# Optimization experiments

Hardware: AMD Instinct MI355X
Metric: run time of the kernel (lower is better)

Reference implementation:

```python
import jax, jax.numpy as jnp
import numpy as np

H = 1024        # hidden_size
E = 3           # num_smear experts
DI = 1280       # int(1.25 * H), GRU inner dim (expansion_factor=1.25)
EPS = 1e-6


def setup_inputs() -> dict:
    key = jax.random.key(0)
    ks = jax.random.split(key, 5)
    B, S = 4, 4096
    s = 0.02
    return {
        "inputs": jax.random.normal(ks[0], (B, S, H), jnp.float32),
        "norm_weight": jnp.ones((H,), jnp.float32),
        "router_w": jax.random.normal(ks[1], (H, E), jnp.float32) * s,
        "router_b": jnp.zeros((E,), jnp.float32),
        "w_in": jax.random.normal(ks[2], (E, H, 2 * DI), jnp.float32) * s,
        "b_in": jnp.zeros((E, 2 * DI), jnp.float32),
        "w_out": jax.random.normal(ks[3], (E, DI, H), jnp.float32) * s,
        "b_out": jnp.zeros((E, H), jnp.float32),
    }


def _g(x):
    # minGRU candidate activation: x + 0.5 for x >= 0, sigmoid(x) otherwise
    return jnp.where(x >= 0, x + 0.5, jax.nn.sigmoid(x))


def reference(inputs, norm_weight, router_w, router_b, w_in, b_in, w_out, b_out):
    B, S, _ = inputs.shape
    # RMSNorm
    x = inputs * jax.lax.rsqrt(jnp.mean(inputs * inputs, axis=-1, keepdims=True) + EPS)
    x = x * norm_weight

    # SMEAR routing: softmax over experts from mean-pooled tokens, per sample
    pooled = x.mean(axis=1)                                   # [B, H]
    probs = jax.nn.softmax(pooled @ router_w + router_b, -1)  # [B, E]

    # Soft-merge expert parameters per sample
    Wi = jnp.einsum('be,edh->bdh', probs, w_in)    # [B, H, 2*DI]
    bi = jnp.einsum('be,eh->bh', probs, b_in)      # [B, 2*DI]
    Wo = jnp.einsum('be,edh->bdh', probs, w_out)   # [B, DI, H]
    bo = jnp.einsum('be,eh->bh', probs, b_out)     # [B, H]

    # GRU (minGRU) input projection
    zh = jnp.einsum('bsd,bdh->bsh', x, Wi) + bi[:, None, :]   # [B, S, 2*DI]
    hid, gate = jnp.split(zh, 2, axis=-1)
    z = jax.nn.sigmoid(gate)   # update gate [B, S, DI]
    ht = _g(hid)               # candidate    [B, S, DI]

    def step(h, zt_ht):
        z_t, ht_t = zt_ht
        h = (1.0 - z_t) * h + z_t * ht_t
        return h, h

    h0 = jnp.zeros((B, DI), x.dtype)
    _, hs = jax.lax.scan(step, h0, (z.swapaxes(0, 1), ht.swapaxes(0, 1)))
    hs = hs.swapaxes(0, 1)     # [B, S, DI]

    out = jnp.einsum('bsh,bhd->bsd', hs, Wo) + bo[:, None, :]  # proj_out
    out = out + inputs                                          # residual (dropout=0, eval)
    new_state = hs[:, -1]                                       # [B, DI]
    aux_loss = jnp.zeros((), inputs.dtype)
    return out, new_state, aux_loss
```

## Files before the change

kernel.cpp:

```cpp
#include <hip/hip_runtime.h>
#include <hip/hip_bf16.h>

#define B_  4
#define S_  4096
#define H_  1024
#define DI_ 1280
#define DI2_ 2560
#define E_  3
#define NC_ 64
#define CL_ 64
#define EPS_ 1e-6f

typedef unsigned short ushort_t;
typedef __attribute__((ext_vector_type(8))) __bf16 bf16x8;
typedef __attribute__((ext_vector_type(4))) float f32x4;

__device__ inline ushort_t f2bf(float f) {
    union { float f; unsigned u; } v; v.f = f;
    unsigned r = v.u + 0x7fffu + ((v.u >> 16) & 1u);
    return (ushort_t)(r >> 16);
}
__device__ inline float bf2f(ushort_t s) {
    union { unsigned u; float f; } v; v.u = ((unsigned)s) << 16;
    return v.f;
}
__device__ inline float sigmoidf_(float x) { return 1.0f / (1.0f + __expf(-x)); }

__device__ inline void gld16(const void* g, void* l) {
    __builtin_amdgcn_global_load_lds(
        (const __attribute__((address_space(1))) void*)g,
        (__attribute__((address_space(3))) void*)l, 16, 0, 0);
}

__global__ __launch_bounds__(256) void rmsnorm_kernel(
    const float* __restrict__ in, const float* __restrict__ nw,
    ushort_t* __restrict__ xbf, float* __restrict__ partial)
{
    int g = blockIdx.x, b = blockIdx.y;
    int tid = threadIdx.x, lane = tid & 63, w = tid >> 6;
    int s0 = g * 16;
    const float4* inb = (const float4*)(in + ((size_t)b * S_ + s0) * H_);
    float4 rows[16];
    float ss[16];
#pragma unroll
    for (int r = 0; r < 16; r++) {
        float4 v = inb[(size_t)r * (H_ / 4) + tid];
        rows[r] = v;
        ss[r] = v.x * v.x + v.y * v.y + v.z * v.z + v.w * v.w;
    }
#pragma unroll
    for (int r = 0; r < 16; r++) {
        float s = ss[r];
        s += __shfl_down(s, 32); s += __shfl_down(s, 16); s += __shfl_down(s, 8);
        s += __shfl_down(s, 4);  s += __shfl_down(s, 2);  s += __shfl_down(s, 1);
        ss[r] = s;
    }
    __shared__ float red[16][4];
    __shared__ float scl[16];
    if (lane == 0) {
#pragma unroll
        for (int r = 0; r < 16; r++) red[r][w] = ss[r];
    }
    __syncthreads();
    if (tid < 16) {
        float t = red[tid][0] + red[tid][1] + red[tid][2] + red[tid][3];
        scl[tid] = rsqrtf(t * (1.0f / H_) + EPS_);
    }
    __syncthreads();
    float4 nw4 = ((const float4*)nw)[tid];
    float4 pacc = {0.f, 0.f, 0.f, 0.f};
    ushort_t* xrow = xbf + ((size_t)b * S_ + s0) * H_;
#pragma unroll
    for (int r = 0; r < 16; r++) {
        float sc = scl[r];
        float4 v = rows[r];
        v.x = v.x * sc * nw4.x; v.y = v.y * sc * nw4.y;
        v.z = v.z * sc * nw4.z; v.w = v.w * sc * nw4.w;
        ushort4 u; u.x = f2bf(v.x); u.y = f2bf(v.y); u.z = f2bf(v.z); u.w = f2bf(v.w);
        *(ushort4*)(xrow + (size_t)r * H_ + tid * 4) = u;
        pacc.x += v.x; pacc.y += v.y; pacc.z += v.z; pacc.w += v.w;
    }
    float4* pp = (float4*)(partial + ((size_t)(b * 256 + g)) * H_);
    pp[tid] = pacc;
}

__global__ __launch_bounds__(256) void router_kernel(
    const float* __restrict__ partial, const float* __restrict__ rw,
    const float* __restrict__ rb, const float* __restrict__ b_in,
    const float* __restrict__ b_out, float* __restrict__ probs,
    float* __restrict__ bi, float* __restrict__ bo, float* __restrict__ aux)
{
    int b = blockIdx.x;
    int tid = threadIdx.x, lane = tid & 63, w = tid >> 6;
    float4 acc = {0.f, 0.f, 0.f, 0.f};
    const float4* pp = (const float4*)partial;
    for (int g = 0; g < 256; g++) {
        float4 v = pp[((size_t)(b * 256 + g)) * (H_ / 4) + tid];
        acc.x += v.x; acc.y += v.y; acc.z += v.z; acc.w += v.w;
    }
    const float inv_s = 1.0f / (float)S_;
    float a4[4] = {acc.x * inv_s, acc.y * inv_s, acc.z * inv_s, acc.w * inv_s};
    float le[3] = {0.f, 0.f, 0.f};
    int h0 = tid * 4;
#pragma unroll
    for (int j = 0; j < 4; j++) {
        float p = a4[j];
        le[0] += p * rw[(size_t)(h0 + j) * 3 + 0];
        le[1] += p * rw[(size_t)(h0 + j) * 3 + 1];
        le[2] += p * rw[(size_t)(h0 + j) * 3 + 2];
    }
#pragma unroll
    for (int e = 0; e < 3; e++) {
        float s = le[e];
        s += __shfl_down(s, 32); s += __shfl_down(s, 16); s += __shfl_down(s, 8);
        s += __shfl_down(s, 4);  s += __shfl_down(s, 2);  s += __shfl_down(s, 1);
        le[e] = s;
    }
    __shared__ float red[4][3];
    __shared__ float pr[3];
    if (lane == 0) { red[w][0] = le[0]; red[w][1] = le[1]; red[w][2] = le[2]; }
    __syncthreads();
    if (tid == 0) {
        float l0 = red[0][0] + red[1][0] + red[2][0] + red[3][0] + rb[0];
        float l1 = red[0][1] + red[1][1] + red[2][1] + red[3][1] + rb[1];
        float l2 = red[0][2] + red[1][2] + red[2][2] + red[3][2] + rb[2];
        float m = fmaxf(l0, fmaxf(l1, l2));
        float e0 = __expf(l0 - m), e1 = __expf(l1 - m), e2 = __expf(l2 - m);
        float inv = 1.0f / (e0 + e1 + e2);
        pr[0] = e0 * inv; pr[1] = e1 * inv; pr[2] = e2 * inv;
    }
    __syncthreads();
    if (tid < 3) probs[b * 3 + tid] = pr[tid];
    float p0 = pr[0], p1 = pr[1], p2 = pr[2];
    for (int n = tid; n < DI2_; n += 256)
        bi[(size_t)b * DI2_ + n] = p0 * b_in[n] + p1 * b_in[DI2_ + n] + p2 * b_in[2 * DI2_ + n];
    for (int n = tid; n < H_; n += 256)
        bo[(size_t)b * H_ + n] = p0 * b_out[n] + p1 * b_out[H_ + n] + p2 * b_out[2 * H_ + n];
    if (b == 0 && tid == 0) *aux = 0.0f;
}

__global__ __launch_bounds__(256) void mix_kernel(
    const float* __restrict__ wsrc, const float* __restrict__ probs,
    ushort_t* __restrict__ dst, int K, int N)
{
    int kt = blockIdx.x, nt = blockIdx.y, b = blockIdx.z;
    float p0 = probs[b * 3 + 0], p1 = probs[b * 3 + 1], p2 = probs[b * 3 + 2];
    __shared__ float T[64][65];
    int tid = threadIdx.x;
    int c = tid & 63, rr = tid >> 6;
    const float* w0 = wsrc;
    const float* w1 = wsrc + (size_t)K * N;
    const float* w2 = wsrc + 2 * (size_t)K * N;
    int k0 = kt * 64, n0 = nt * 64;
#pragma unroll
    for (int pass = 0; pass < 16; pass++) {
        int r = pass * 4 + rr;
        size_t idx = (size_t)(k0 + r) * N + n0 + c;
        T[r][c] = p0 * w0[idx] + p1 * w1[idx] + p2 * w2[idx];
    }
    __syncthreads();
    ushort_t* db = dst + (size_t)b * N * K;
#pragma unroll
    for (int pass = 0; pass < 16; pass++) {
        int j = pass * 4 + rr;
        db[(size_t)(n0 + j) * K + k0 + c] = f2bf(T[c][j]);
    }
}

template <int MODE>
__global__ __launch_bounds__(256, 2) void gemm_bt(
    const ushort_t* __restrict__ Aall, const ushort_t* __restrict__ Btall,
    int M, int N, int K,
    const float* __restrict__ biasAll,
    const float* __restrict__ resAll, float* __restrict__ outAll,
    ushort_t* __restrict__ htAll, ushort_t* __restrict__ zAll, int DIv)
{
    __shared__ ushort_t As[128 * 32];
    __shared__ ushort_t Bs[128 * 32];
    int b = blockIdx.z;
    const ushort_t* A = Aall + (size_t)b * M * K;
    const ushort_t* Bt = Btall + (size_t)b * N * K;
    int tid = threadIdx.x, lane = tid & 63, w = tid >> 6;
    int mblk = blockIdx.x * 128, nblk = blockIdx.y * 128;

    int srow = lane >> 2;
    int scol = (lane & 3) * 8;
    const ushort_t* ga0 = A + (size_t)(mblk + (w * 2 + 0) * 16 + srow) * K + scol;
    const ushort_t* ga1 = A + (size_t)(mblk + (w * 2 + 1) * 16 + srow) * K + scol;
    const ushort_t* gb0 = Bt + (size_t)(nblk + (w * 2 + 0) * 16 + srow) * K + scol;
    const ushort_t* gb1 = Bt + (size_t)(nblk + (w * 2 + 1) * 16 + srow) * K + scol;
    ushort_t* la0 = &As[(w * 2 + 0) * 512 + lane * 8];
    ushort_t* la1 = &As[(w * 2 + 1) * 512 + lane * 8];
    ushort_t* lb0 = &Bs[(w * 2 + 0) * 512 + lane * 8];
    ushort_t* lb1 = &Bs[(w * 2 + 1) * 512 + lane * 8];

    f32x4 acc[4][4] = {};
    int wy = w & 1, wx = w >> 1;
    int q = lane >> 4;
    int ml = lane & 15;
    int aoff0 = (wy * 64 + ml) * 32 + q * 8;
    int boff0 = (wx * 64 + ml) * 32 + q * 8;

    for (int k0 = 0; k0 < K; k0 += 32) {
        gld16(ga0, la0); gld16(ga1, la1);
        gld16(gb0, lb0); gld16(gb1, lb1);
        ga0 += 32; ga1 += 32; gb0 += 32; gb1 += 32;
        __syncthreads();
        bf16x8 af[4], bfr[4];
#pragma unroll
        for (int i = 0; i < 4; i++) af[i] = *(const bf16x8*)&As[aoff0 + i * 16 * 32];
#pragma unroll
        for (int i = 0; i < 4; i++) bfr[i] = *(const bf16x8*)&Bs[boff0 + i * 16 * 32];
#pragma unroll
        for (int mi = 0; mi < 4; mi++)
#pragma unroll
            for (int ni = 0; ni < 4; ni++)
                acc[mi][ni] = __builtin_amdgcn_mfma_f32_16x16x32_bf16(af[mi], bfr[ni], acc[mi][ni], 0, 0, 0);
        __syncthreads();
    }

    int mbase = mblk + wy * 64 + q * 4;
    int nbase = nblk + wx * 64 + ml;
    const float* bias = biasAll + (size_t)b * N;
    if (MODE == 0) {
        bool isgate = (nblk >= DIv);
        ushort_t* dst = (isgate ? zAll : htAll) + (size_t)b * (size_t)M * DIv;
#pragma unroll
        for (int ni = 0; ni < 4; ni++) {
            int n = nbase + ni * 16;
            float bv = bias[n];
            int ncol = isgate ? (n - DIv) : n;
#pragma unroll
            for (int mi = 0; mi < 4; mi++) {
                int m = mbase + mi * 16;
#pragma unroll
                for (int r = 0; r < 4; r++) {
                    float v = acc[mi][ni][r] + bv;
                    float res;
                    if (isgate) res = sigmoidf_(v);
                    else res = (v >= 0.f) ? (v + 0.5f) : sigmoidf_(v);
                    dst[(size_t)(m + r) * DIv + ncol] = f2bf(res);
                }
            }
        }
    } else {
        const float* resb = resAll + (size_t)b * (size_t)M * N;
        float* outp = outAll + (size_t)b * (size_t)M * N;
#pragma unroll
        for (int ni = 0; ni < 4; ni++) {
            int n = nbase + ni * 16;
            float bv = bias[n];
#pragma unroll
            for (int mi = 0; mi < 4; mi++) {
                int m = mbase + mi * 16;
#pragma unroll
                for (int r = 0; r < 4; r++) {
                    size_t idx = (size_t)(m + r) * N + n;
                    outp[idx] = acc[mi][ni][r] + bv + resb[idx];
                }
            }
        }
    }
}

__global__ __launch_bounds__(256) void scan_phase1(
    const ushort_t* __restrict__ zb, const ushort_t* __restrict__ hb,
    float* __restrict__ cA, float* __restrict__ cB)
{
    int d = blockIdx.x * 256 + threadIdx.x;
    int c = blockIdx.y, b = blockIdx.z;
    size_t base = ((size_t)b * S_ + (size_t)c * CL_) * DI_ + d;
    float A = 1.f, Bc = 0.f;
    for (int t = 0; t < CL_; t++) {
        float z = bf2f(zb[base + (size_t)t * DI_]);
        float h = bf2f(hb[base + (size_t)t * DI_]);
        float a = 1.f - z;
        A *= a;
        Bc = a * Bc + z * h;
    }
    size_t o = ((size_t)b * NC_ + c) * DI_ + d;
    cA[o] = A;
    cB[o] = Bc;
}

__global__ __launch_bounds__(256) void scan_phase2(
    const float* __restrict__ cA, const float* __restrict__ cB,
    float* __restrict__ h0buf, float* __restrict__ ns)
{
    int g = blockIdx.x * 256 + threadIdx.x;
    int b = g / DI_, d = g % DI_;
    float h = 0.f;
    for (int c = 0; c < NC_; c++) {
        size_t o = ((size_t)b * NC_ + c) * DI_ + d;
        h0buf[o] = h;
        h = cA[o] * h + cB[o];
    }
    ns[(size_t)b * DI_ + d] = h;
}

__global__ __launch_bounds__(256) void scan_phase3(
    const ushort_t* __restrict__ zb, const ushort_t* __restrict__ hb,
    const float* __restrict__ h0buf, ushort_t* __restrict__ hs)
{
    int d = blockIdx.x * 256 + threadIdx.x;
    int c = blockIdx.y, b = blockIdx.z;
    size_t base = ((size_t)b * S_ + (size_t)c * CL_) * DI_ + d;
    float h = h0buf[((size_t)b * NC_ + c) * DI_ + d];
    for (int t = 0; t < CL_; t++) {
        float z = bf2f(zb[base + (size_t)t * DI_]);
        float ht = bf2f(hb[base + (size_t)t * DI_]);
        h = (1.f - z) * h + z * ht;
        hs[base + (size_t)t * DI_] = f2bf(h);
    }
}

extern "C" void kernel_launch(void* const* d_in, const int* in_sizes, int n_in,
                              void* d_out, int out_size, void* d_ws, size_t ws_size,
                              hipStream_t stream)
{
    const float* in    = (const float*)d_in[0];
    const float* nw    = (const float*)d_in[1];
    const float* rw    = (const float*)d_in[2];
    const float* rb    = (const float*)d_in[3];
    const float* w_in  = (const float*)d_in[4];
    const float* b_in  = (const float*)d_in[5];
    const float* w_out = (const float*)d_in[6];
    const float* b_out = (const float*)d_in[7];
    float* out = (float*)d_out;

    char* ws = (char*)d_ws;
    size_t off = 0;
    auto nxt = [&](size_t bytes) -> void* {
        void* p = ws + off;
        off += (bytes + 255) & ~(size_t)255;
        return p;
    };
    ushort_t* xbf    = (ushort_t*)nxt((size_t)B_ * S_ * H_ * 2);
    ushort_t* wi_t   = (ushort_t*)nxt((size_t)B_ * DI2_ * H_ * 2);
    ushort_t* wo_t   = (ushort_t*)nxt((size_t)B_ * H_ * DI_ * 2);
    ushort_t* zbuf   = (ushort_t*)nxt((size_t)B_ * S_ * DI_ * 2);
    ushort_t* htbuf  = (ushort_t*)nxt((size_t)B_ * S_ * DI_ * 2);
    ushort_t* hsbuf  = (ushort_t*)nxt((size_t)B_ * S_ * DI_ * 2);
    float* partial   = (float*)nxt((size_t)B_ * 256 * H_ * 4);
    float* probs     = (float*)nxt((size_t)B_ * 3 * 4);
    float* bi        = (float*)nxt((size_t)B_ * DI2_ * 4);
    float* bo        = (float*)nxt((size_t)B_ * H_ * 4);
    float* cA        = (float*)nxt((size_t)B_ * NC_ * DI_ * 4);
    float* cB        = (float*)nxt((size_t)B_ * NC_ * DI_ * 4);
    float* h0buf     = (float*)nxt((size_t)B_ * NC_ * DI_ * 4);

    float* ns  = out + (size_t)B_ * S_ * H_;
    float* aux = ns + (size_t)B_ * DI_;

    rmsnorm_kernel<<<dim3(S_ / 16, B_), 256, 0, stream>>>(in, nw, xbf, partial);
    router_kernel<<<dim3(B_), 256, 0, stream>>>(partial, rw, rb, b_in, b_out, probs, bi, bo, aux);
    mix_kernel<<<dim3(H_ / 64, DI2_ / 64, B_), 256, 0, stream>>>(w_in, probs, wi_t, H_, DI2_);
    mix_kernel<<<dim3(DI_ / 64, H_ / 64, B_), 256, 0, stream>>>(w_out, probs, wo_t, DI_, H_);
    gemm_bt<0><<<dim3(S_ / 128, DI2_ / 128, B_), 256, 0, stream>>>(
        xbf, wi_t, S_, DI2_, H_, bi, nullptr, nullptr, htbuf, zbuf, DI_);
    scan_phase1<<<dim3(DI_ / 256, NC_, B_), 256, 0, stream>>>(zbuf, htbuf, cA, cB);
    scan_phase2<<<dim3((B_ * DI_) / 256), 256, 0, stream>>>(cA, cB, h0buf, ns);
    scan_phase3<<<dim3(DI_ / 256, NC_, B_), 256, 0, stream>>>(zbuf, htbuf, h0buf, hsbuf);
    gemm_bt<1><<<dim3(S_ / 128, H_ / 128, B_), 256, 0, stream>>>(
        hsbuf, wo_t, S_, H_, DI_, bo, in, out, nullptr, nullptr, DI_);
    (void)in_sizes; (void)n_in; (void)out_size; (void)ws_size;
}
```

Measured before the change: 463.7 us.

## Swizzle GEMM LDS layout, vectorize epilogue stores and scan kernels

The GEMM stages its shared-memory tiles with an XOR swizzle to avoid bank conflicts. It also swaps the MFMA operand order so each lane holds four consecutive output columns, which lets the epilogue use vector stores for the bf16 and fp32 outputs and vector loads for the residual and bias. The three scan phases now process four channels per thread with vector loads and stores, using fewer, wider blocks. The scan grids shrink, so phase2 runs only 5 blocks and phases 1 and 3 run 256 blocks, which may leave much of the GPU idle.

```diff
diff --git a/kernel.cpp b/kernel.cpp
--- a/kernel.cpp
+++ b/kernel.cpp
@@ -184,7 +184,8 @@
     int mblk = blockIdx.x * 128, nblk = blockIdx.y * 128;
 
     int srow = lane >> 2;
-    int scol = (lane & 3) * 8;
+    int sblk = (lane & 3) ^ ((srow >> 1) & 3);
+    int scol = sblk * 8;
     const ushort_t* ga0 = A + (size_t)(mblk + (w * 2 + 0) * 16 + srow) * K + scol;
     const ushort_t* ga1 = A + (size_t)(mblk + (w * 2 + 1) * 16 + srow) * K + scol;
     const ushort_t* gb0 = Bt + (size_t)(nblk + (w * 2 + 0) * 16 + srow) * K + scol;
@@ -198,8 +199,9 @@
     int wy = w & 1, wx = w >> 1;
     int q = lane >> 4;
     int ml = lane & 15;
-    int aoff0 = (wy * 64 + ml) * 32 + q * 8;
-    int boff0 = (wx * 64 + ml) * 32 + q * 8;
+    int rblk = (q ^ ((ml >> 1) & 3)) * 8;
+    int aoff0 = wy * 2048 + ml * 32 + rblk;
+    int boff0 = wx * 2048 + ml * 32 + rblk;
 
     for (int k0 = 0; k0 < K; k0 += 32) {
         gld16(ga0, la0); gld16(ga1, la1);
@@ -208,79 +210,94 @@
         __syncthreads();
         bf16x8 af[4], bfr[4];
 #pragma unroll
-        for (int i = 0; i < 4; i++) af[i] = *(const bf16x8*)&As[aoff0 + i * 16 * 32];
-#pragma unroll
-        for (int i = 0; i < 4; i++) bfr[i] = *(const bf16x8*)&Bs[boff0 + i * 16 * 32];
+        for (int i = 0; i < 4; i++) af[i] = *(const bf16x8*)&As[aoff0 + i * 512];
+#pragma unroll
+        for (int i = 0; i < 4; i++) bfr[i] = *(const bf16x8*)&Bs[boff0 + i * 512];
 #pragma unroll
         for (int mi = 0; mi < 4; mi++)
 #pragma unroll
             for (int ni = 0; ni < 4; ni++)
-                acc[mi][ni] = __builtin_amdgcn_mfma_f32_16x16x32_bf16(af[mi], bfr[ni], acc[mi][ni], 0, 0, 0);
+                acc[mi][ni] = __builtin_amdgcn_mfma_f32_16x16x32_bf16(bfr[ni], af[mi], acc[mi][ni], 0, 0, 0);
         __syncthreads();
     }
 
-    int mbase = mblk + wy * 64 + q * 4;
-    int nbase = nblk + wx * 64 + ml;
+    int nq = nblk + wx * 64 + q * 4;
     const float* bias = biasAll + (size_t)b * N;
     if (MODE == 0) {
         bool isgate = (nblk >= DIv);
         ushort_t* dst = (isgate ? zAll : htAll) + (size_t)b * (size_t)M * DIv;
-#pragma unroll
-        for (int ni = 0; ni < 4; ni++) {
-            int n = nbase + ni * 16;
-            float bv = bias[n];
-            int ncol = isgate ? (n - DIv) : n;
-#pragma unroll
-            for (int mi = 0; mi < 4; mi++) {
-                int m = mbase + mi * 16;
-#pragma unroll
-                for (int r = 0; r < 4; r++) {
-                    float v = acc[mi][ni][r] + bv;
-                    float res;
-                    if (isgate) res = sigmoidf_(v);
-                    else res = (v >= 0.f) ? (v + 0.5f) : sigmoidf_(v);
-                    dst[(size_t)(m + r) * DIv + ncol] = f2bf(res);
+        int ncol0 = isgate ? (nq - DIv) : nq;
+#pragma unroll
+        for (int mi = 0; mi < 4; mi++) {
+            int m = mblk + wy * 64 + mi * 16 + ml;
+            ushort_t* drow = dst + (size_t)m * DIv;
+#pragma unroll
+            for (int ni = 0; ni < 4; ni++) {
+                float4 bv = *(const float4*)&bias[nq + ni * 16];
+                f32x4 a = acc[mi][ni];
+                float v0 = a[0] + bv.x, v1 = a[1] + bv.y, v2 = a[2] + bv.z, v3 = a[3] + bv.w;
+                float r0, r1, r2, r3;
+                if (isgate) {
+                    r0 = sigmoidf_(v0); r1 = sigmoidf_(v1); r2 = sigmoidf_(v2); r3 = sigmoidf_(v3);
+                } else {
+                    r0 = (v0 >= 0.f) ? (v0 + 0.5f) : sigmoidf_(v0);
+                    r1 = (v1 >= 0.f) ? (v1 + 0.5f) : sigmoidf_(v1);
+                    r2 = (v2 >= 0.f) ? (v2 + 0.5f) : sigmoidf_(v2);
+                    r3 = (v3 >= 0.f) ? (v3 + 0.5f) : sigmoidf_(v3);
                 }
+                ushort4 u; u.x = f2bf(r0); u.y = f2bf(r1); u.z = f2bf(r2); u.w = f2bf(r3);
+                *(ushort4*)&drow[ncol0 + ni * 16] = u;
             }
         }
     } else {
         const float* resb = resAll + (size_t)b * (size_t)M * N;
         float* outp = outAll + (size_t)b * (size_t)M * N;
 #pragma unroll
-        for (int ni = 0; ni < 4; ni++) {
-            int n = nbase + ni * 16;
-            float bv = bias[n];
-#pragma unroll
-            for (int mi = 0; mi < 4; mi++) {
-                int m = mbase + mi * 16;
-#pragma unroll
-                for (int r = 0; r < 4; r++) {
-                    size_t idx = (size_t)(m + r) * N + n;
-                    outp[idx] = acc[mi][ni][r] + bv + resb[idx];
-                }
+        for (int mi = 0; mi < 4; mi++) {
+            int m = mblk + wy * 64 + mi * 16 + ml;
+            const float* rrow = resb + (size_t)m * N;
+            float* orow = outp + (size_t)m * N;
+#pragma unroll
+            for (int ni = 0; ni < 4; ni++) {
+                int n0 = nq + ni * 16;
+                float4 bv = *(const float4*)&bias[n0];
+                float4 rv = *(const float4*)&rrow[n0];
+                f32x4 a = acc[mi][ni];
+                float4 o;
+                o.x = a[0] + bv.x + rv.x; o.y = a[1] + bv.y + rv.y;
+                o.z = a[2] + bv.z + rv.z; o.w = a[3] + bv.w + rv.w;
+                *(float4*)&orow[n0] = o;
             }
         }
     }
 }
 
-__global__ __launch_bounds__(256) void scan_phase1(
+__global__ __launch_bounds__(320) void scan_phase1(
     const ushort_t* __restrict__ zb, const ushort_t* __restrict__ hb,
     float* __restrict__ cA, float* __restrict__ cB)
 {
-    int d = blockIdx.x * 256 + threadIdx.x;
-    int c = blockIdx.y, b = blockIdx.z;
-    size_t base = ((size_t)b * S_ + (size_t)c * CL_) * DI_ + d;
-    float A = 1.f, Bc = 0.f;
+    int d0 = threadIdx.x * 4;
+    int c = blockIdx.x, b = blockIdx.y;
+    size_t base = ((size_t)b * S_ + (size_t)c * CL_) * DI_ + d0;
+    float A[4] = {1.f, 1.f, 1.f, 1.f};
+    float Bc[4] = {0.f, 0.f, 0.f, 0.f};
     for (int t = 0; t < CL_; t++) {
-        float z = bf2f(zb[base + (size_t)t * DI_]);
-        float h = bf2f(hb[base + (size_t)t * DI_]);
-        float a = 1.f - z;
-        A *= a;
-        Bc = a * Bc + z * h;
-    }
-    size_t o = ((size_t)b * NC_ + c) * DI_ + d;
-    cA[o] = A;
-    cB[o] = Bc;
+        ushort4 zv = *(const ushort4*)&zb[base + (size_t)t * DI_];
+        ushort4 hv = *(const ushort4*)&hb[base + (size_t)t * DI_];
+        float z[4] = {bf2f(zv.x), bf2f(zv.y), bf2f(zv.z), bf2f(zv.w)};
+        float h[4] = {bf2f(hv.x), bf2f(hv.y), bf2f(hv.z), bf2f(hv.w)};
+#pragma unroll
+        for (int j = 0; j < 4; j++) {
+            float a = 1.f - z[j];
+            A[j] *= a;
+            Bc[j] = a * Bc[j] + z[j] * h[j];
+        }
+    }
+    size_t o = ((size_t)b * NC_ + c) * DI_ + d0;
+    float4 av; av.x = A[0]; av.y = A[1]; av.z = A[2]; av.w = A[3];
+    float4 bv; bv.x = Bc[0]; bv.y = Bc[1]; bv.z = Bc[2]; bv.w = Bc[3];
+    *(float4*)&cA[o] = av;
+    *(float4*)&cB[o] = bv;
 }
 
 __global__ __launch_bounds__(256) void scan_phase2(
@@ -288,29 +305,40 @@
     float* __restrict__ h0buf, float* __restrict__ ns)
 {
     int g = blockIdx.x * 256 + threadIdx.x;
-    int b = g / DI_, d = g % DI_;
-    float h = 0.f;
+    int b = g / (DI_ / 4), dq = g % (DI_ / 4);
+    int d0 = dq * 4;
+    float4 h = {0.f, 0.f, 0.f, 0.f};
     for (int c = 0; c < NC_; c++) {
-        size_t o = ((size_t)b * NC_ + c) * DI_ + d;
-        h0buf[o] = h;
-        h = cA[o] * h + cB[o];
-    }
-    ns[(size_t)b * DI_ + d] = h;
-}
-
-__global__ __launch_bounds__(256) void scan_phase3(
+        size_t o = ((size_t)b * NC_ + c) * DI_ + d0;
+        *(float4*)&h0buf[o] = h;
+        float4 a = *(const float4*)&cA[o];
+        float4 bb = *(const float4*)&cB[o];
+        h.x = a.x * h.x + bb.x; h.y = a.y * h.y + bb.y;
+        h.z = a.z * h.z + bb.z; h.w = a.w * h.w + bb.w;
+    }
+    *(float4*)&ns[(size_t)b * DI_ + d0] = h;
+}
+
+__global__ __launch_bounds__(320) void scan_phase3(
     const ushort_t* __restrict__ zb, const ushort_t* __restrict__ hb,
     const float* __restrict__ h0buf, ushort_t* __restrict__ hs)
 {
-    int d = blockIdx.x * 256 + threadIdx.x;
-    int c = blockIdx.y, b = blockIdx.z;
-    size_t base = ((size_t)b * S_ + (size_t)c * CL_) * DI_ + d;
-    float h = h0buf[((size_t)b * NC_ + c) * DI_ + d];
+    int d0 = threadIdx.x * 4;
+    int c = blockIdx.x, b = blockIdx.y;
+    size_t base = ((size_t)b * S_ + (size_t)c * CL_) * DI_ + d0;
+    float4 h0 = *(const float4*)&h0buf[((size_t)b * NC_ + c) * DI_ + d0];
+    float h[4] = {h0.x, h0.y, h0.z, h0.w};
     for (int t = 0; t < CL_; t++) {
-        float z = bf2f(zb[base + (size_t)t * DI_]);
-        float ht = bf2f(hb[base + (size_t)t * DI_]);
-        h = (1.f - z) * h + z * ht;
-        hs[base + (size_t)t * DI_] = f2bf(h);
+        ushort4 zv = *(const ushort4*)&zb[base + (size_t)t * DI_];
+        ushort4 hv = *(const ushort4*)&hb[base + (size_t)t * DI_];
+        float z[4] = {bf2f(zv.x), bf2f(zv.y), bf2f(zv.z), bf2f(zv.w)};
+        float ht[4] = {bf2f(hv.x), bf2f(hv.y), bf2f(hv.z), bf2f(hv.w)};
+        ushort4 u;
+        h[0] = (1.f - z[0]) * h[0] + z[0] * ht[0]; u.x = f2bf(h[0]);
+        h[1] = (1.f - z[1]) * h[1] + z[1] * ht[1]; u.y = f2bf(h[1]);
+        h[2] = (1.f - z[2]) * h[2] + z[2] * ht[2]; u.z = f2bf(h[2]);
+        h[3] = (1.f - z[3]) * h[3] + z[3] * ht[3]; u.w = f2bf(h[3]);
+        *(ushort4*)&hs[base + (size_t)t * DI_] = u;
     }
 }
 
@@ -358,9 +386,9 @@
     mix_kernel<<<dim3(DI_ / 64, H_ / 64, B_), 256, 0, stream>>>(w_out, probs, wo_t, DI_, H_);
     gemm_bt<0><<<dim3(S_ / 128, DI2_ / 128, B_), 256, 0, stream>>>(
         xbf, wi_t, S_, DI2_, H_, bi, nullptr, nullptr, htbuf, zbuf, DI_);
-    scan_phase1<<<dim3(DI_ / 256, NC_, B_), 256, 0, stream>>>(zbuf, htbuf, cA, cB);
-    scan_phase2<<<dim3((B_ * DI_) / 256), 256, 0, stream>>>(cA, cB, h0buf, ns);
-    scan_phase3<<<dim3(DI_ / 256, NC_, B_), 256, 0, stream>>>(zbuf, htbuf, h0buf, hsbuf);
+    scan_phase1<<<dim3(NC_, B_), 320, 0, stream>>>(zbuf, htbuf, cA, cB);
+    scan_phase2<<<dim3(5), 256, 0, stream>>>(cA, cB, h0buf, ns);
+    scan_phase3<<<dim3(NC_, B_), 320, 0, stream>>>(zbuf, htbuf, h0buf, hsbuf);
     gemm_bt<1><<<dim3(S_ / 128, H_ / 128, B_), 256, 0, stream>>>(
         hsbuf, wo_t, S_, H_, DI_, bo, in, out, nullptr, nullptr, DI_);
     (void)in_sizes; (void)n_in; (void)out_size; (void)ws_size;
```

After: 436.2 us. 5.9% less time.
